# Performance work log

Hardware: AMD Instinct MI355X
Metric: run time of the kernel (lower is better)

## Reference

```python
import jax, jax.numpy as jnp
import numpy as np

N_NODES = 100000
N_EDGES = 20000
N_INC = 800000


def hconv(node_idx, edge_idx, X, w, W, b):
    # node -> hyperedge: weighted mean of member node features
    msg = X[node_idx] * w[node_idx, None]                      # [I, d]
    e_sum = jax.ops.segment_sum(msg, edge_idx, num_segments=N_EDGES)
    e_den = jax.ops.segment_sum(w[node_idx], edge_idx, num_segments=N_EDGES)
    e_feat = e_sum / jnp.maximum(e_den, 1e-6)[:, None]         # [E, d]
    # hyperedge -> node: mean over incident hyperedges
    v_sum = jax.ops.segment_sum(e_feat[edge_idx], node_idx, num_segments=N_NODES)
    v_deg = jax.ops.segment_sum(jnp.ones((edge_idx.shape[0],), X.dtype),
                                node_idx, num_segments=N_NODES)
    v_feat = v_sum / jnp.maximum(v_deg, 1.0)[:, None]          # [N, d]
    return v_feat @ W + b


def setup_inputs() -> dict:
    key = jax.random.key(0)
    k1, k2, k3, k4, k5, k6 = jax.random.split(key, 6)
    d, h, c = 256, 16, 40
    H = jax.random.normal(k1, (N_NODES, d), dtype=jnp.float32)
    input_weight = jax.random.uniform(k2, (N_NODES,), dtype=jnp.float32)
    node_idx = jax.random.randint(k3, (N_INC,), 0, N_NODES, dtype=jnp.int32)
    edge_idx = jax.random.randint(k4, (N_INC,), 0, N_EDGES, dtype=jnp.int32)
    W1 = jax.random.normal(k5, (d, h), dtype=jnp.float32) / np.sqrt(d)
    b1 = jnp.zeros((h,), jnp.float32)
    W2 = jax.random.normal(k6, (h, c), dtype=jnp.float32) / np.sqrt(h)
    b2 = jnp.zeros((c,), jnp.float32)
    return {"H": H, "input_weight": input_weight, "node_idx": node_idx,
            "edge_idx": edge_idx, "W1": W1, "b1": b1, "W2": W2, "b2": b2}


def reference(H, input_weight, node_idx, edge_idx, W1, b1, W2, b2):
    x = jax.nn.relu(hconv(node_idx, edge_idx, H, input_weight, W1, b1))
    # dropout is identity at inference (training=False)
    x = hconv(node_idx, edge_idx, x, input_weight, W2, b2)
    return jax.nn.log_softmax(x, axis=1)
```

## Files before the change

kernel.cpp:

```cpp
#include <hip/hip_runtime.h>

#define N_NODES 100000
#define N_EDGES 20000
#define N_INC   800000
#define D_IN    256
#define D_H     16
#define D_OUT   40

#define EBS    32
#define NBE    625
#define ECAP   1600
#define VBS    256
#define NBV    392
#define VCAP   2400
#define TE     4096
#define EPART  196
#define TV     6144
#define NPART  131
#define PTOT   327
#define GEMM_BLOCKS 782
#define GRID_K1 1120

typedef short bf16x8 __attribute__((ext_vector_type(8)));
typedef float f32x4  __attribute__((ext_vector_type(4)));

__device__ __forceinline__ unsigned short f2bf(float f) {
    unsigned u = __float_as_uint(f);
    unsigned r = u + 0x7FFF + ((u >> 16) & 1);
    return (unsigned short)(r >> 16);
}

__device__ __forceinline__ int block_exscan512(int local, int* sc8) {
    int t = threadIdx.x, lane = t & 63, wid = t >> 6;
    int s = local;
#pragma unroll
    for (int o = 1; o < 64; o <<= 1) {
        int x = __shfl_up(s, o, 64);
        if (lane >= o) s += x;
    }
    if (lane == 63) sc8[wid] = s;
    __syncthreads();
    int wbase = 0;
#pragma unroll
    for (int i = 0; i < 8; ++i) if (i < wid) wbase += sc8[i];
    return wbase + s - local;
}

__global__ __launch_bounds__(512) void init_kernel(
    const float* __restrict__ W1, unsigned short* __restrict__ bfrag,
    int* __restrict__ cnts ) {
    int t = threadIdx.x;
    for (int i = t; i < 1040; i += 512) cnts[i] = 0;
    int c = t >> 6, l = t & 63;
    int n = l & 15, q = l >> 4;
    unsigned short v[8];
#pragma unroll
    for (int j = 0; j < 8; ++j)
        v[j] = f2bf(W1[(c * 32 + q * 8 + j) * D_H + n]);
    *(int4*)(bfrag + (size_t)(c * 64 + l) * 8) = *(int4*)v;
}

union SMemP {
    struct { int lrec[TE]; int lhist[NBE]; int lbase[NBE];
             int gbase[NBE]; int lcur[NBE]; int sc[8]; } pe;
    struct { int lrec[TV]; int lhist[NBV]; int lbase[NBV];
             int gbase[NBV]; int lcur[NBV]; int sc[8]; } pn;
};

__global__ __launch_bounds__(512) void part_gemm_kernel(
    const int* __restrict__ ni, const int* __restrict__ ei,
    const float* __restrict__ w,
    int* __restrict__ cnt_be, int* __restrict__ cnt_bv,
    int* __restrict__ staged_e, int* __restrict__ staged_v,
    const float* __restrict__ H, const unsigned short* __restrict__ bfrag,
    float* __restrict__ T) {
    __shared__ SMemP sm;
    int t = threadIdx.x;
    int m10 = blockIdx.x % 10, g10 = blockIdx.x / 10;
    bool is_part = (m10 < 3);
    int pj = g10 * 3 + m10;
    int gj = g10 * 7 + (m10 - 3);
    if (is_part && pj >= PTOT) return;
    if (!is_part && gj >= GEMM_BLOCKS) return;

    if (!is_part) {
        int wave = (gj * 512 + t) >> 6;
        if (wave >= N_NODES / 16) return;
        int lane = t & 63;
        int m = lane & 15, q = lane >> 4;
        int row0 = wave * 16;
        const float* hp = H + (size_t)(row0 + m) * D_IN + q * 8;
        bf16x8 bf[8];
        const int4* bp = (const int4*)bfrag;
#pragma unroll
        for (int c = 0; c < 8; ++c) {
            int4 raw = bp[c * 64 + lane];
            bf[c] = *(bf16x8*)&raw;
        }
        f32x4 acc = {0.f, 0.f, 0.f, 0.f};
#pragma unroll
        for (int c = 0; c < 8; ++c) {
            float4 lo = *(const float4*)(hp + c * 32);
            float4 hi = *(const float4*)(hp + c * 32 + 4);
            bf16x8 af;
            af[0] = f2bf(lo.x); af[1] = f2bf(lo.y); af[2] = f2bf(lo.z); af[3] = f2bf(lo.w);
            af[4] = f2bf(hi.x); af[5] = f2bf(hi.y); af[6] = f2bf(hi.z); af[7] = f2bf(hi.w);
            acc = __builtin_amdgcn_mfma_f32_16x16x32_bf16(af, bf[c], acc, 0, 0, 0);
        }
#pragma unroll
        for (int r = 0; r < 4; ++r) {
            int row = row0 + q * 4 + r;
            T[(size_t)row * D_H + m] = acc[r] * w[row];
        }
    } else if (pj < EPART) {
        int base = pj * TE;
        int rec[TE / 512];
        for (int i = t; i < NBE; i += 512) sm.pe.lhist[i] = 0;
        __syncthreads();
#pragma unroll
        for (int r = 0; r < TE / 512; ++r) {
            int idx = base + r * 512 + t;
            rec[r] = -1;
            if (idx < N_INC) {
                int e = ei[idx], v = ni[idx];
                int key = e >> 5;
                rec[r] = v | ((e & 31) << 17) | (key << 22);
                atomicAdd(&sm.pe.lhist[key], 1);
            }
        }
        __syncthreads();
        int b0 = 2 * t, b1 = 2 * t + 1;
        int h0 = (b0 < NBE) ? sm.pe.lhist[b0] : 0;
        int h1 = (b1 < NBE) ? sm.pe.lhist[b1] : 0;
        int ex = block_exscan512(h0 + h1, sm.pe.sc);
        if (b0 < NBE) {
            sm.pe.lbase[b0] = ex; sm.pe.lcur[b0] = ex;
            sm.pe.gbase[b0] = h0 ? (b0 * ECAP + atomicAdd(&cnt_be[b0], h0)) : 0;
        }
        if (b1 < NBE) {
            int ex1 = ex + h0;
            sm.pe.lbase[b1] = ex1; sm.pe.lcur[b1] = ex1;
            sm.pe.gbase[b1] = h1 ? (b1 * ECAP + atomicAdd(&cnt_be[b1], h1)) : 0;
        }
        __syncthreads();
#pragma unroll
        for (int r = 0; r < TE / 512; ++r) {
            if (rec[r] != -1) {
                int key = ((unsigned)rec[r]) >> 22;
                int p = atomicAdd(&sm.pe.lcur[key], 1);
                sm.pe.lrec[p] = rec[r];
            }
        }
        __syncthreads();
        int total = min(TE, N_INC - base);
        for (int i = t; i < total; i += 512) {
            int rr = sm.pe.lrec[i];
            int bk = ((unsigned)rr) >> 22;
            int dst = sm.pe.gbase[bk] + (i - sm.pe.lbase[bk]);
            if (dst < (bk + 1) * ECAP) staged_e[dst] = rr;
        }
    } else {
        int base = (pj - EPART) * TV;
        int rec[TV / 512];
        for (int i = t; i < NBV; i += 512) sm.pn.lhist[i] = 0;
        __syncthreads();
#pragma unroll
        for (int r = 0; r < TV / 512; ++r) {
            int idx = base + r * 512 + t;
            rec[r] = -1;
            if (idx < N_INC) {
                int e = ei[idx], v = ni[idx];
                int key = v >> 8;
                rec[r] = e | ((v & 255) << 15) | (key << 23);
                atomicAdd(&sm.pn.lhist[key], 1);
            }
        }
        __syncthreads();
        int h = (t < NBV) ? sm.pn.lhist[t] : 0;
        int ex = block_exscan512(h, sm.pn.sc);
        if (t < NBV) {
            sm.pn.lbase[t] = ex; sm.pn.lcur[t] = ex;
            sm.pn.gbase[t] = h ? (t * VCAP + atomicAdd(&cnt_bv[t], h)) : 0;
        }
        __syncthreads();
#pragma unroll
        for (int r = 0; r < TV / 512; ++r) {
            if (rec[r] != -1) {
                int key = ((unsigned)rec[r]) >> 23;
                int p = atomicAdd(&sm.pn.lcur[key], 1);
                sm.pn.lrec[p] = rec[r];
            }
        }
        __syncthreads();
        int total = min(TV, N_INC - base);
        for (int i = t; i < total; i += 512) {
            int rr = sm.pn.lrec[i];
            int bk = ((unsigned)rr) >> 23;
            int dst = sm.pn.gbase[bk] + (i - sm.pn.lbase[bk]);
            if (dst < (bk + 1) * VCAP) staged_v[dst] = rr;
        }
    }
}

union SMemS {
    struct { int lsort[ECAP]; int hist[EBS]; int cursor[EBS]; int lbeg[EBS]; } e;
    struct { int lsort[VCAP]; int hist[VBS]; int cursor[VBS]; int sc[8]; } v;
};

__global__ __launch_bounds__(512) void sortE_gA1_sortN_kernel(
    const int* __restrict__ cnt_be, int* __restrict__ staged_e,
    int2* __restrict__ off_e2,
    const int* __restrict__ cnt_bv, int* __restrict__ staged_v,
    int2* __restrict__ off_v2,
    const float* __restrict__ T, const float* __restrict__ w,
    float* __restrict__ e_den, float* __restrict__ e_feat) {
    __shared__ SMemS sm;
    int t = threadIdx.x;
    if (blockIdx.x < NBE) {
        int b = blockIdx.x;
        int beg = b * ECAP, cnt = min(cnt_be[b], ECAP);
        if (t < EBS) sm.e.hist[t] = 0;
        __syncthreads();
        int rec[4], key[4], nr = 0;
#pragma unroll
        for (int r = 0; r < 4; ++r) {
            int k = r * 512 + t;
            if (k < cnt) {
                rec[nr] = staged_e[beg + k];
                key[nr] = (rec[nr] >> 17) & 31;
                atomicAdd(&sm.e.hist[key[nr]], 1);
                ++nr;
            }
        }
        __syncthreads();
        if (t < EBS) {
            int hh = sm.e.hist[t], s = hh;
#pragma unroll
            for (int o = 1; o < EBS; o <<= 1) {
                int x = __shfl_up(s, o, 64);
                if (t >= o) s += x;
            }
            int ex = s - hh;
            sm.e.cursor[t] = ex; sm.e.lbeg[t] = ex;
            off_e2[b * EBS + t] = make_int2(beg + ex, beg + ex + hh);
        }
        __syncthreads();
        for (int r = 0; r < nr; ++r) {
            int p = atomicAdd(&sm.e.cursor[key[r]], 1);
            sm.e.lsort[p] = rec[r];
        }
        __syncthreads();
        for (int i = t; i < cnt; i += 512) staged_e[beg + i] = sm.e.lsort[i];
        int el = t >> 4, j = t & 15;
        int lo = sm.e.lbeg[el], hi = lo + sm.e.hist[el];
        float acc = 0.f;
        int k = lo;
        for (; k + 4 <= hi; k += 4) {
            int r0 = sm.e.lsort[k]     & 0x1FFFF;
            int r1 = sm.e.lsort[k + 1] & 0x1FFFF;
            int r2 = sm.e.lsort[k + 2] & 0x1FFFF;
            int r3 = sm.e.lsort[k + 3] & 0x1FFFF;
            float t0 = T[(size_t)r0 * D_H + j];
            float t1 = T[(size_t)r1 * D_H + j];
            float t2 = T[(size_t)r2 * D_H + j];
            float t3 = T[(size_t)r3 * D_H + j];
            acc += t0; acc += t1; acc += t2; acc += t3;
        }
        for (; k < hi; ++k) acc += T[(size_t)(sm.e.lsort[k] & 0x1FFFF) * D_H + j];
        float den = 0.f;
        for (int k2 = lo + j; k2 < hi; k2 += 16) den += w[sm.e.lsort[k2] & 0x1FFFF];
#pragma unroll
        for (int o = 1; o < 16; o <<= 1) den += __shfl_xor(den, o, 64);
        int e = b * EBS + el;
        e_feat[(size_t)e * D_H + j] = acc / fmaxf(den, 1e-6f);
        if (j == 0) e_den[e] = den;
    } else {
        int b = blockIdx.x - NBE;
        int beg = b * VCAP, cnt = min(cnt_bv[b], VCAP);
        for (int i = t; i < VBS; i += 512) sm.v.hist[i] = 0;
        __syncthreads();
        int rec[5], key[5], nr = 0;
#pragma unroll
        for (int r = 0; r < 5; ++r) {
            int k = r * 512 + t;
            if (k < cnt) {
                rec[nr] = staged_v[beg + k];
                key[nr] = (rec[nr] >> 15) & 255;
                atomicAdd(&sm.v.hist[key[nr]], 1);
                ++nr;
            }
        }
        __syncthreads();
        int hh = (t < VBS) ? sm.v.hist[t] : 0;
        int ex = block_exscan512(hh, sm.v.sc);
        if (t < VBS) {
            sm.v.cursor[t] = ex;
            int n = b * VBS + t;
            if (n < N_NODES) off_v2[n] = make_int2(beg + ex, beg + ex + hh);
        }
        __syncthreads();
        for (int r = 0; r < nr; ++r) {
            int p = atomicAdd(&sm.v.cursor[key[r]], 1);
            sm.v.lsort[p] = rec[r];
        }
        __syncthreads();
        for (int i = t; i < cnt; i += 512) staged_v[beg + i] = sm.v.lsort[i];
    }
}

__global__ __launch_bounds__(512) void gatherB1_kernel(
    const int2* __restrict__ off_v2, const int* __restrict__ staged_v,
    const float* __restrict__ e_feat, const float* __restrict__ w,
    const float* __restrict__ b1, float* __restrict__ out) {
    int t = blockIdx.x * 512 + threadIdx.x;
    int n = t >> 2;
    if (n >= N_NODES) return;
    int c = (t & 3) << 2;
    int2 be = off_v2[n];
    f32x4 acc = {0.f, 0.f, 0.f, 0.f};
    for (int k = be.x; k < be.y; ++k) {
        int e = staged_v[k] & 0x7FFF;
        acc += *(const f32x4*)(e_feat + (size_t)e * D_H + c);
    }
    float inv = 1.f / fmaxf((float)(be.y - be.x), 1.f);
    f32x4 bb = *(const f32x4*)(b1 + c);
    float wn = w[n];
    f32x4 r;
#pragma unroll
    for (int i = 0; i < 4; ++i) r[i] = fmaxf(acc[i] * inv + bb[i], 0.f) * wn;
    *(f32x4*)(out + (size_t)n * D_H + c) = r;
}

__global__ __launch_bounds__(512) void gatherA2_kernel(
    const int2* __restrict__ off_e2, const int* __restrict__ staged_e,
    const float* __restrict__ X, const float* __restrict__ e_den,
    float* __restrict__ e_feat) {
    int e = (blockIdx.x * 512 + threadIdx.x) >> 6;
    if (e >= N_EDGES) return;
    int lane = threadIdx.x & 63;
    int g = lane >> 2, c = (lane & 3) << 2;
    int2 be = off_e2[e];
    f32x4 acc = {0.f, 0.f, 0.f, 0.f};
    for (int k = be.x + g; k < be.y; k += 16) {
        int rec = staged_e[k];
        int v = rec & 0x1FFFF;
        acc += *(const f32x4*)(X + (size_t)v * D_H + c);
    }
#pragma unroll
    for (int s = 4; s <= 32; s <<= 1) {
        acc[0] += __shfl_xor(acc[0], s, 64);
        acc[1] += __shfl_xor(acc[1], s, 64);
        acc[2] += __shfl_xor(acc[2], s, 64);
        acc[3] += __shfl_xor(acc[3], s, 64);
    }
    if (lane < 4) {
        float inv = 1.f / fmaxf(e_den[e], 1e-6f);
        f32x4 r = acc * inv;
        *(f32x4*)(e_feat + (size_t)e * D_H + c) = r;
    }
}

__global__ __launch_bounds__(512) void gatherB2_final_kernel(
    const int2* __restrict__ off_v2, const int* __restrict__ staged_v,
    const float* __restrict__ e_feat,
    const float* __restrict__ W2, const float* __restrict__ b2,
    float* __restrict__ out) {
    __shared__ float sy[128 * 20];
    __shared__ float sW2[D_H * D_OUT];
    __shared__ float sb2[D_OUT];
    int t = threadIdx.x;
    for (int i = t; i < D_H * D_OUT; i += 512) sW2[i] = W2[i];
    if (t < D_OUT) sb2[t] = b2[t];
    int nl = t >> 2, c = (t & 3) << 2;
    int n = blockIdx.x * 128 + nl;
    f32x4 y = {0.f, 0.f, 0.f, 0.f};
    if (n < N_NODES) {
        int2 be = off_v2[n];
        f32x4 acc = {0.f, 0.f, 0.f, 0.f};
        for (int k = be.x; k < be.y; ++k) {
            int e = staged_v[k] & 0x7FFF;
            acc += *(const f32x4*)(e_feat + (size_t)e * D_H + c);
        }
        float inv = 1.f / fmaxf((float)(be.y - be.x), 1.f);
        y = acc * inv;
    }
    *(f32x4*)(sy + nl * 20 + c) = y;
    __syncthreads();
    if (n >= N_NODES) return;
    int c0 = (t & 3) * 10;
    float z[10];
#pragma unroll
    for (int i = 0; i < 10; ++i) z[i] = sb2[c0 + i];
#pragma unroll
    for (int jj = 0; jj < D_H; ++jj) {
        float yy = sy[nl * 20 + jj];
#pragma unroll
        for (int i = 0; i < 10; ++i) z[i] += yy * sW2[jj * D_OUT + c0 + i];
    }
    float m = z[0];
#pragma unroll
    for (int i = 1; i < 10; ++i) m = fmaxf(m, z[i]);
    m = fmaxf(m, __shfl_xor(m, 1, 64));
    m = fmaxf(m, __shfl_xor(m, 2, 64));
    float se = 0.f;
#pragma unroll
    for (int i = 0; i < 10; ++i) se += __expf(z[i] - m);
    se += __shfl_xor(se, 1, 64);
    se += __shfl_xor(se, 2, 64);
    float lse = m + __logf(se);
    float* op = out + (size_t)n * D_OUT + c0;
#pragma unroll
    for (int i = 0; i < 10; ++i) op[i] = z[i] - lse;
}

extern "C" void kernel_launch(void* const* d_in, const int* in_sizes, int n_in,
                              void* d_out, int out_size, void* d_ws, size_t ws_size,
                              hipStream_t stream) {
    const float* H  = (const float*)d_in[0];
    const float* w  = (const float*)d_in[1];
    const int*   ni = (const int*)d_in[2];
    const int*   ei = (const int*)d_in[3];
    const float* W1 = (const float*)d_in[4];
    const float* b1 = (const float*)d_in[5];
    const float* W2 = (const float*)d_in[6];
    const float* b2 = (const float*)d_in[7];
    float* out = (float*)d_out;

    int*            ws_i     = (int*)d_ws;
    int*            cnt_be   = ws_i + 0;
    int*            cnt_bv   = ws_i + 640;
    unsigned short* bfrag    = (unsigned short*)(ws_i + 1040);
    int2*           off_e2   = (int2*)(ws_i + 3088);
    int2*           off_v2   = (int2*)(ws_i + 43088);
    int*            staged_e = ws_i + 243088;
    int*            staged_v = ws_i + 1243088;
    float*          e_den    = (float*)(ws_i + 2183888);
    float*          T        = (float*)(ws_i + 2203888);
    float*          e_feat   = (float*)(ws_i + 3803888);
    float*          x1       = (float*)(ws_i + 4123888);

    init_kernel<<<1, 512, 0, stream>>>(W1, bfrag, cnt_be);

    part_gemm_kernel<<<GRID_K1, 512, 0, stream>>>(
        ni, ei, w, cnt_be, cnt_bv, staged_e, staged_v, H, bfrag, T);

    sortE_gA1_sortN_kernel<<<NBE + NBV, 512, 0, stream>>>(
        cnt_be, staged_e, off_e2, cnt_bv, staged_v, off_v2, T, w, e_den, e_feat);

    gatherB1_kernel<<<782, 512, 0, stream>>>(off_v2, staged_v, e_feat, w, b1, x1);

    gatherA2_kernel<<<2500, 512, 0, stream>>>(off_e2, staged_e, x1, e_den, e_feat);

    gatherB2_final_kernel<<<782, 512, 0, stream>>>(
        off_v2, staged_v, e_feat, W2, b2, out);
}
```

Baseline: 242.4 us.

## Split fused partition/GEMM kernel, pad bucket counters, hoist GEMM loads

Splits the interleaved partition+GEMM kernel into separate partition and GEMM launches. The bucket counters are padded to 16 ints (64 bytes) apart so global atomics from different blocks hit separate cache lines. The GEMM now issues all 16 float4 loads of H up front, before any conversion or MFMA, to expose more memory-level parallelism. The trade-off is an extra kernel launch and the loss of overlap between the partition and GEMM blocks.

Measured after the change: 252.6 us. 4.2% more time.

```diff
diff --git a/kernel.cpp b/kernel.cpp
--- a/kernel.cpp
+++ b/kernel.cpp
@@ -19,7 +19,7 @@
 #define NPART  131
 #define PTOT   327
 #define GEMM_BLOCKS 782
-#define GRID_K1 1120
+#define CPAD   16
 
 typedef short bf16x8 __attribute__((ext_vector_type(8)));
 typedef float f32x4  __attribute__((ext_vector_type(4)));
@@ -50,7 +50,7 @@
     const float* __restrict__ W1, unsigned short* __restrict__ bfrag,
     int* __restrict__ cnts ) {
     int t = threadIdx.x;
-    for (int i = t; i < 1040; i += 512) cnts[i] = 0;
+    for (int i = t; i < (NBE + NBV) * CPAD; i += 512) cnts[i] = 0;
     int c = t >> 6, l = t & 63;
     int n = l & 15, q = l >> 4;
     unsigned short v[8];
@@ -67,53 +67,14 @@
              int gbase[NBV]; int lcur[NBV]; int sc[8]; } pn;
 };
 
-__global__ __launch_bounds__(512) void part_gemm_kernel(
+__global__ __launch_bounds__(512) void part_kernel(
     const int* __restrict__ ni, const int* __restrict__ ei,
-    const float* __restrict__ w,
     int* __restrict__ cnt_be, int* __restrict__ cnt_bv,
-    int* __restrict__ staged_e, int* __restrict__ staged_v,
-    const float* __restrict__ H, const unsigned short* __restrict__ bfrag,
-    float* __restrict__ T) {
+    int* __restrict__ staged_e, int* __restrict__ staged_v) {
     __shared__ SMemP sm;
     int t = threadIdx.x;
-    int m10 = blockIdx.x % 10, g10 = blockIdx.x / 10;
-    bool is_part = (m10 < 3);
-    int pj = g10 * 3 + m10;
-    int gj = g10 * 7 + (m10 - 3);
-    if (is_part && pj >= PTOT) return;
-    if (!is_part && gj >= GEMM_BLOCKS) return;
-
-    if (!is_part) {
-        int wave = (gj * 512 + t) >> 6;
-        if (wave >= N_NODES / 16) return;
-        int lane = t & 63;
-        int m = lane & 15, q = lane >> 4;
-        int row0 = wave * 16;
-        const float* hp = H + (size_t)(row0 + m) * D_IN + q * 8;
-        bf16x8 bf[8];
-        const int4* bp = (const int4*)bfrag;
-#pragma unroll
-        for (int c = 0; c < 8; ++c) {
-            int4 raw = bp[c * 64 + lane];
-            bf[c] = *(bf16x8*)&raw;
-        }
-        f32x4 acc = {0.f, 0.f, 0.f, 0.f};
-#pragma unroll
-        for (int c = 0; c < 8; ++c) {
-            float4 lo = *(const float4*)(hp + c * 32);
-            float4 hi = *(const float4*)(hp + c * 32 + 4);
-            bf16x8 af;
-            af[0] = f2bf(lo.x); af[1] = f2bf(lo.y); af[2] = f2bf(lo.z); af[3] = f2bf(lo.w);
-            af[4] = f2bf(hi.x); af[5] = f2bf(hi.y); af[6] = f2bf(hi.z); af[7] = f2bf(hi.w);
-            acc = __builtin_amdgcn_mfma_f32_16x16x32_bf16(af, bf[c], acc, 0, 0, 0);
-        }
-#pragma unroll
-        for (int r = 0; r < 4; ++r) {
-            int row = row0 + q * 4 + r;
-            T[(size_t)row * D_H + m] = acc[r] * w[row];
-        }
-    } else if (pj < EPART) {
-        int base = pj * TE;
+    if (blockIdx.x < EPART) {
+        int base = blockIdx.x * TE;
         int rec[TE / 512];
         for (int i = t; i < NBE; i += 512) sm.pe.lhist[i] = 0;
         __syncthreads();
@@ -135,12 +96,12 @@
         int ex = block_exscan512(h0 + h1, sm.pe.sc);
         if (b0 < NBE) {
             sm.pe.lbase[b0] = ex; sm.pe.lcur[b0] = ex;
-            sm.pe.gbase[b0] = h0 ? (b0 * ECAP + atomicAdd(&cnt_be[b0], h0)) : 0;
+            sm.pe.gbase[b0] = h0 ? (b0 * ECAP + atomicAdd(&cnt_be[b0 * CPAD], h0)) : 0;
         }
         if (b1 < NBE) {
             int ex1 = ex + h0;
             sm.pe.lbase[b1] = ex1; sm.pe.lcur[b1] = ex1;
-            sm.pe.gbase[b1] = h1 ? (b1 * ECAP + atomicAdd(&cnt_be[b1], h1)) : 0;
+            sm.pe.gbase[b1] = h1 ? (b1 * ECAP + atomicAdd(&cnt_be[b1 * CPAD], h1)) : 0;
         }
         __syncthreads();
 #pragma unroll
@@ -160,7 +121,7 @@
             if (dst < (bk + 1) * ECAP) staged_e[dst] = rr;
         }
     } else {
-        int base = (pj - EPART) * TV;
+        int base = (blockIdx.x - EPART) * TV;
         int rec[TV / 512];
         for (int i = t; i < NBV; i += 512) sm.pn.lhist[i] = 0;
         __syncthreads();
@@ -180,7 +141,7 @@
         int ex = block_exscan512(h, sm.pn.sc);
         if (t < NBV) {
             sm.pn.lbase[t] = ex; sm.pn.lcur[t] = ex;
-            sm.pn.gbase[t] = h ? (t * VCAP + atomicAdd(&cnt_bv[t], h)) : 0;
+            sm.pn.gbase[t] = h ? (t * VCAP + atomicAdd(&cnt_bv[t * CPAD], h)) : 0;
         }
         __syncthreads();
 #pragma unroll
@@ -199,6 +160,45 @@
             int dst = sm.pn.gbase[bk] + (i - sm.pn.lbase[bk]);
             if (dst < (bk + 1) * VCAP) staged_v[dst] = rr;
         }
+    }
+}
+
+__global__ __launch_bounds__(512) void gemm_kernel(
+    const float* __restrict__ H, const unsigned short* __restrict__ bfrag,
+    const float* __restrict__ w, float* __restrict__ T) {
+    int wave = (blockIdx.x * 512 + threadIdx.x) >> 6;
+    if (wave >= N_NODES / 16) return;
+    int lane = threadIdx.x & 63;
+    int m = lane & 15, q = lane >> 4;
+    int row0 = wave * 16;
+    const float4* hp = (const float4*)(H + (size_t)(row0 + m) * D_IN) + q * 2;
+
+    float4 la[16];
+#pragma unroll
+    for (int c = 0; c < 8; ++c) {
+        la[2 * c]     = hp[c * 8];
+        la[2 * c + 1] = hp[c * 8 + 1];
+    }
+    bf16x8 bf[8];
+    const int4* bp = (const int4*)bfrag;
+#pragma unroll
+    for (int c = 0; c < 8; ++c) {
+        int4 raw = bp[c * 64 + lane];
+        bf[c] = *(bf16x8*)&raw;
+    }
+    f32x4 acc = {0.f, 0.f, 0.f, 0.f};
+#pragma unroll
+    for (int c = 0; c < 8; ++c) {
+        float4 lo = la[2 * c], hi = la[2 * c + 1];
+        bf16x8 af;
+        af[0] = f2bf(lo.x); af[1] = f2bf(lo.y); af[2] = f2bf(lo.z); af[3] = f2bf(lo.w);
+        af[4] = f2bf(hi.x); af[5] = f2bf(hi.y); af[6] = f2bf(hi.z); af[7] = f2bf(hi.w);
+        acc = __builtin_amdgcn_mfma_f32_16x16x32_bf16(af, bf[c], acc, 0, 0, 0);
+    }
+#pragma unroll
+    for (int r = 0; r < 4; ++r) {
+        int row = row0 + q * 4 + r;
+        T[(size_t)row * D_H + m] = acc[r] * w[row];
     }
 }
 
@@ -218,7 +218,7 @@
     int t = threadIdx.x;
     if (blockIdx.x < NBE) {
         int b = blockIdx.x;
-        int beg = b * ECAP, cnt = min(cnt_be[b], ECAP);
+        int beg = b * ECAP, cnt = min(cnt_be[b * CPAD], ECAP);
         if (t < EBS) sm.e.hist[t] = 0;
         __syncthreads();
         int rec[4], key[4], nr = 0;
@@ -276,7 +276,7 @@
         if (j == 0) e_den[e] = den;
     } else {
         int b = blockIdx.x - NBE;
-        int beg = b * VCAP, cnt = min(cnt_bv[b], VCAP);
+        int beg = b * VCAP, cnt = min(cnt_bv[b * CPAD], VCAP);
         for (int i = t; i < VBS; i += 512) sm.v.hist[i] = 0;
         __syncthreads();
         int rec[5], key[5], nr = 0;
@@ -428,21 +428,23 @@
 
     int*            ws_i     = (int*)d_ws;
     int*            cnt_be   = ws_i + 0;
-    int*            cnt_bv   = ws_i + 640;
-    unsigned short* bfrag    = (unsigned short*)(ws_i + 1040);
-    int2*           off_e2   = (int2*)(ws_i + 3088);
-    int2*           off_v2   = (int2*)(ws_i + 43088);
-    int*            staged_e = ws_i + 243088;
-    int*            staged_v = ws_i + 1243088;
-    float*          e_den    = (float*)(ws_i + 2183888);
-    float*          T        = (float*)(ws_i + 2203888);
-    float*          e_feat   = (float*)(ws_i + 3803888);
-    float*          x1       = (float*)(ws_i + 4123888);
+    int*            cnt_bv   = ws_i + 10000;
+    unsigned short* bfrag    = (unsigned short*)(ws_i + 16272);
+    int2*           off_e2   = (int2*)(ws_i + 18320);
+    int2*           off_v2   = (int2*)(ws_i + 58320);
+    int*            staged_e = ws_i + 258320;
+    int*            staged_v = ws_i + 1258320;
+    float*          e_den    = (float*)(ws_i + 2199120);
+    float*          T        = (float*)(ws_i + 2219120);
+    float*          e_feat   = (float*)(ws_i + 3819120);
+    float*          x1       = (float*)(ws_i + 4139120);
 
     init_kernel<<<1, 512, 0, stream>>>(W1, bfrag, cnt_be);
 
-    part_gemm_kernel<<<GRID_K1, 512, 0, stream>>>(
-        ni, ei, w, cnt_be, cnt_bv, staged_e, staged_v, H, bfrag, T);
+    part_kernel<<<PTOT, 512, 0, stream>>>(ni, ei, cnt_be, cnt_bv,
+                                          staged_e, staged_v);
+
+    gemm_kernel<<<GEMM_BLOCKS, 512, 0, stream>>>(H, bfrag, w, T);
 
     sortE_gA1_sortN_kernel<<<NBE + NBV, 512, 0, stream>>>(
         cnt_be, staged_e, off_e2, cnt_bv, staged_v, off_v2, T, w, e_den, e_feat);
```
